# Optimization experiments

Measured on AMD Instinct MI355X. Metric: run time of the kernel, lower is better.

Reference implementation:

```python
import jax, jax.numpy as jnp
import numpy as np
from jax import lax

B, D, H, W = 4, 64, 64, 64
CH = 150


def setup_inputs() -> dict:
    key = jax.random.key(0)
    k1, k2, k3, k4 = jax.random.split(key, 4)
    image = jax.random.uniform(k1, (B, 2, D, H, W), dtype=jnp.float32)
    # PyTorch-like init scales
    h_w = jax.random.normal(k2, (CH, 1, 3, 3, 3), dtype=jnp.float32) * (1.0 / np.sqrt(27.0))
    h_b = jax.random.normal(k3, (CH,), dtype=jnp.float32) * 0.05
    p_w = jax.random.normal(k4, (1, CH, 1, 1, 1), dtype=jnp.float32) * (1.0 / np.sqrt(CH))
    return {"image": image, "h_w": h_w, "h_b": h_b, "p_w": p_w, "k": 30}


def _max_pool3(v):
    # 3x3x3 max pool, stride 1, padding 1 (torch pads with -inf for max pool)
    return lax.reduce_window(
        v, -jnp.inf, lax.max,
        window_dimensions=(1, 1, 3, 3, 3),
        window_strides=(1, 1, 1, 1, 1),
        padding=[(0, 0), (0, 0), (1, 1), (1, 1), (1, 1)])


def reference(image, h_w, h_b, p_w, k):
    x = image[:, 0:1]            # [B,1,D,H,W] occupancy
    r = image[:, 1:2]            # [B,1,D,H,W] reward
    h = lax.conv_general_dilated(
        x, h_w, window_strides=(1, 1, 1), padding="SAME",
        dimension_numbers=("NCDHW", "OIDHW", "NCDHW"))
    h = jax.nn.relu(h + h_b[None, :, None, None, None])  # [B,150,D,H,W]
    # 1x1x1 conv == channel contraction
    p = jax.nn.sigmoid(jnp.einsum("bcdhw,c->bdhw", h, p_w[0, :, 0, 0, 0])[:, None])
    v = r
    for _ in range(k):
        v = jnp.maximum(v, r + p * (_max_pool3(v) - r))
    return v
```

## Files before the change

kernel.cpp:

```cpp
#include <hip/hip_runtime.h>
#include <math.h>

#define NEG_INF (-__builtin_inff())

typedef __attribute__((ext_vector_type(8))) short short8;
typedef __attribute__((ext_vector_type(4))) float f32x4;

__device__ __forceinline__ unsigned f2bf(float f) {
    union { float f; unsigned u; } v; v.f = f;
    return (v.u + 0x7fffu + ((v.u >> 16) & 1u)) >> 16;
}

__device__ __forceinline__ float dpp_shr1(float x) {
    return __int_as_float(__builtin_amdgcn_update_dpp(
        0, __float_as_int(x), 0x111, 0xF, 0xF, true));
}
__device__ __forceinline__ float dpp_shr2(float x) {
    return __int_as_float(__builtin_amdgcn_update_dpp(
        0, __float_as_int(x), 0x112, 0xF, 0xF, true));
}
__device__ __forceinline__ float dpp_shr4(float x) {
    return __int_as_float(__builtin_amdgcn_update_dpp(
        0, __float_as_int(x), 0x114, 0xF, 0xF, true));
}
__device__ __forceinline__ float dpp_shr8(float x) {
    return __int_as_float(__builtin_amdgcn_update_dpp(
        0, __float_as_int(x), 0x118, 0xF, 0xF, true));
}
__device__ __forceinline__ float dpp_shl1(float x) {
    return __int_as_float(__builtin_amdgcn_update_dpp(
        0, __float_as_int(x), 0x101, 0xF, 0xF, true));
}

__global__ __launch_bounds__(256) void pad_kernel(
    const float* __restrict__ img, unsigned short* __restrict__ pad)
{
    int i = blockIdx.x * 256 + threadIdx.x;
    if (i >= 66 * 66 * 66) return;
    int b = blockIdx.y;
    int z = i / 4356;
    int rem = i - z * 4356;
    int y = rem / 66;
    int x = rem - y * 66;
    float v = 0.f;
    if (z >= 1 && z <= 64 && y >= 1 && y <= 64 && x >= 1 && x <= 64)
        v = img[((size_t)b << 19) + ((z - 1) << 12) + ((y - 1) << 6) + (x - 1)];
    pad[(size_t)b * 287496 + i] = (unsigned short)f2bf(v);
}

__global__ __launch_bounds__(256, 4) void gate_mfma(
    const unsigned short* __restrict__ pad,
    const float* __restrict__ hw, const float* __restrict__ hb,
    const float* __restrict__ pw, float* __restrict__ p)
{
    __shared__ int4 Bsh[10 * 64];

    const int lane = threadIdx.x & 63;
    const int col  = lane & 15;
    const int q    = lane >> 4;
    const int wid  = threadIdx.x >> 6;
    const int W    = blockIdx.x * 4 + wid;

    for (int t = wid; t < 10; t += 4) {
        int c = 16 * t + col;
        bool cv = c < 150;
        unsigned hv[8];
        #pragma unroll
        for (int j = 0; j < 8; ++j) {
            int k = 8 * q + j;
            float wv = 0.f;
            if (cv) {
                if (k < 27) wv = hw[c * 27 + k];
                else if (k == 27) wv = hb[c];
            }
            hv[j] = f2bf(wv);
        }
        Bsh[t * 64 + lane] = make_int4(hv[0] | (hv[1] << 16), hv[2] | (hv[3] << 16),
                                       hv[4] | (hv[5] << 16), hv[6] | (hv[7] << 16));
    }
    float pwv[10];
    #pragma unroll
    for (int t = 0; t < 10; ++t) {
        int c = 16 * t + col;
        pwv[t] = (c < 150) ? pw[c] : 0.f;
    }
    __syncthreads();

    int4 bfrag[10];
    #pragma unroll
    for (int t = 0; t < 10; ++t) bfrag[t] = Bsh[t * 64 + lane];

    int offL[8]; unsigned cstA[8]; bool ldA[8];
    #pragma unroll
    for (int j = 0; j < 8; ++j) {
        int k = 8 * q + j;
        int dz = (k * 57) >> 9;
        int rem = k - 9 * dz;
        int dy = (rem * 171) >> 9;
        int dx = rem - 3 * dy;
        ldA[j]  = (k < 27);
        offL[j] = (k < 27) ? (dz * 4356 + dy * 66 + dx) : 0;
        cstA[j] = (k == 27) ? 0x3F80u : 0u;
    }

    int y = W & 63, zz = (W >> 6) & 63, b = W >> 12;
    int rbase = b * 287496 + zz * 4356 + y * 66 + col;

    #pragma unroll 2
    for (int i = 0; i < 4; ++i) {
        int x0    = i << 4;
        int abase = rbase + x0;

        unsigned av[8];
        #pragma unroll
        for (int j = 0; j < 8; ++j) {
            unsigned v = pad[abase + offL[j]];
            av[j] = ldA[j] ? v : cstA[j];
        }
        union { int4 i4; short8 s8; } af, bfu;
        af.i4 = make_int4(av[0] | (av[1] << 16), av[2] | (av[3] << 16),
                          av[4] | (av[5] << 16), av[6] | (av[7] << 16));

        const f32x4 zero = {0.f, 0.f, 0.f, 0.f};
        f32x4 rr[10];
        #pragma unroll
        for (int t = 0; t < 10; ++t) {
            bfu.i4 = bfrag[t];
            rr[t] = __builtin_amdgcn_mfma_f32_16x16x32_bf16(af.s8, bfu.s8, zero, 0, 0, 0);
        }
        float ax = 0.f, ay = 0.f, az = 0.f, aw = 0.f;
        #pragma unroll
        for (int t = 0; t < 10; ++t) {
            ax = fmaf(pwv[t], fmaxf(rr[t].x, 0.f), ax);
            ay = fmaf(pwv[t], fmaxf(rr[t].y, 0.f), ay);
            az = fmaf(pwv[t], fmaxf(rr[t].z, 0.f), az);
            aw = fmaf(pwv[t], fmaxf(rr[t].w, 0.f), aw);
        }
        ax += dpp_shr1(ax); ax += dpp_shr2(ax); ax += dpp_shr4(ax); ax += dpp_shr8(ax);
        ay += dpp_shr1(ay); ay += dpp_shr2(ay); ay += dpp_shr4(ay); ay += dpp_shr8(ay);
        az += dpp_shr1(az); az += dpp_shr2(az); az += dpp_shr4(az); az += dpp_shr8(az);
        aw += dpp_shr1(aw); aw += dpp_shr2(aw); aw += dpp_shr4(aw); aw += dpp_shr8(aw);
        if (col == 15) {
            float4 o;
            o.x = 1.f / (1.f + __expf(-ax));
            o.y = 1.f / (1.f + __expf(-ay));
            o.z = 1.f / (1.f + __expf(-az));
            o.w = 1.f / (1.f + __expf(-aw));
            *(float4*)(p + (b << 18) + (zz << 12) + (y << 6) + x0 + 4 * q) = o;
        }
    }
}

#define ZC 12
#define YC 16
#define PL 1024
#define ZMID 6

template<int T>
__global__ __launch_bounds__(512, 4) void prop_kernel(
    const float* __restrict__ vin, int sstride,
    const float* __restrict__ rimg,
    const float* __restrict__ pbuf,
    float* __restrict__ vout)
{
    __shared__ float S[ZC * PL];
    int blk = blockIdx.x;
    int b  = blk >> 7;
    int tz = ((blk >> 3) & 15) << 2;
    int ty = (blk & 7) << 3;

    const float* vb = vin  + (size_t)b * sstride;
    const float* rb = rimg + ((size_t)b << 19);
    const float* pb = pbuf + ((size_t)b << 18);
    float*       ob = vout + ((size_t)b << 18);

    int tid  = threadIdx.x;
    int x4   = tid & 15, x0 = x4 << 2;
    int yy   = (tid >> 4) & 15;
    int h    = tid >> 8;
    int lane = tid & 63;
    (void)lane;

    int gy = ty + yy - 4;
    bool vy = (unsigned)gy < 64u;

    {
        const float* src = vb + gy * 64 + x0;
        #pragma unroll
        for (int zi = 0; zi < 6; ++zi) {
            int z  = 6 * h + zi;
            int gz = tz + z - 4;
            float4 v = make_float4(NEG_INF, NEG_INF, NEG_INF, NEG_INF);
            if (vy && ((unsigned)gz < 64u)) v = *(const float4*)(src + (gz << 12));
            *(float4*)(S + z * PL + yy * 64 + x0) = v;
        }
    }
    __syncthreads();

    int lbase = yy * 64 + x0;
    int goff  = gy * 64 + x0;

    #define ROWY(zz_, Q, C) {                                                  \
        const float* pz = S + (zz_) * PL + lbase;                              \
        float4 r0 = *(const float4*)(pz - 64);                                 \
        float4 r1 = *(const float4*)(pz);                                      \
        float4 r2 = *(const float4*)(pz + 64);                                 \
        float4 cm;                                                             \
        cm.x = fmaxf(fmaxf(r0.x, r1.x), r2.x);                                 \
        cm.y = fmaxf(fmaxf(r0.y, r1.y), r2.y);                                 \
        cm.z = fmaxf(fmaxf(r0.z, r1.z), r2.z);                                 \
        cm.w = fmaxf(fmaxf(r0.w, r1.w), r2.w);                                 \
        float lm = dpp_shr1(cm.w);                        \
        float rm = dpp_shl1(cm.x);                        \
        if (x4 == 0)  lm = NEG_INF;                                            \
        if (x4 == 15) rm = NEG_INF;                                            \
        Q.x = fmaxf(lm, fmaxf(cm.x, cm.y));                                    \
        Q.y = fmaxf(cm.x, fmaxf(cm.y, cm.z));                                  \
        Q.z = fmaxf(cm.y, fmaxf(cm.z, cm.w));                                  \
        Q.w = fmaxf(fmaxf(cm.z, cm.w), rm);                                    \
        C = r1;                                                                \
    }

    #pragma unroll
    for (int it = 0; it < T; ++it) {
        const int lo   = 5 - T + it;
        const int span = ZMID - lo;
        bool act = (yy >= lo) && (yy < YC - lo);
        int zlo = h ? ZMID : lo;
        float4 vn[5];
        if (act) {
            float4 q0, q1, q2, c1, c2, cd;
            ROWY(zlo - 1, q0, cd);
            ROWY(zlo,     q1, c1);
            #pragma unroll
            for (int zi = 0; zi < span; ++zi) {
                int z = zlo + zi;
                ROWY(z + 1, q2, c2);
                int gz = tz + z - 4;
                float4 r;
                if (vy && ((unsigned)gz < 64u)) {
                    int off = (gz << 12) + goff;
                    float4 pv = *(const float4*)(pb + off);
                    float4 rv = *(const float4*)(rb + off);
                    float4 m3;
                    m3.x = fmaxf(fmaxf(q0.x, q1.x), q2.x);
                    m3.y = fmaxf(fmaxf(q0.y, q1.y), q2.y);
                    m3.z = fmaxf(fmaxf(q0.z, q1.z), q2.z);
                    m3.w = fmaxf(fmaxf(q0.w, q1.w), q2.w);
                    r.x = fmaxf(c1.x, fmaf(pv.x, m3.x - rv.x, rv.x));
                    r.y = fmaxf(c1.y, fmaf(pv.y, m3.y - rv.y, rv.y));
                    r.z = fmaxf(c1.z, fmaf(pv.z, m3.z - rv.z, rv.z));
                    r.w = fmaxf(c1.w, fmaf(pv.w, m3.w - rv.w, rv.w));
                    if (it == T - 1) *(float4*)(ob + off) = r;
                } else {
                    r = c1;
                }
                vn[zi] = r;
                q0 = q1; q1 = q2; c1 = c2;
            }
        }
        __syncthreads();
        if (act) {
            #pragma unroll
            for (int zi = 0; zi < span; ++zi)
                *(float4*)(S + (zlo + zi) * PL + lbase) = vn[zi];
        }
        __syncthreads();
    }
    #undef ROWY
}

extern "C" void kernel_launch(void* const* d_in, const int* in_sizes, int n_in,
                              void* d_out, int out_size, void* d_ws, size_t ws_size,
                              hipStream_t stream) {
    const float* img = (const float*)d_in[0];
    const float* hw  = (const float*)d_in[1];
    const float* hb  = (const float*)d_in[2];
    const float* pw  = (const float*)d_in[3];

    float* out = (float*)d_out;
    float* p   = (float*)d_ws;
    float* vA  = (float*)((char*)d_ws + (4u << 20));
    unsigned short* pad = (unsigned short*)((char*)d_ws + (4u << 20));

    pad_kernel<<<dim3(1124, 4), 256, 0, stream>>>(img, pad);
    gate_mfma<<<4096, 256, 0, stream>>>(pad, hw, hb, pw, p);

    const float* r0 = img + (1 << 18);

    prop_kernel<4><<<512, 512, 0, stream>>>(r0,  1 << 19, r0, p, vA);
    prop_kernel<4><<<512, 512, 0, stream>>>(vA,  1 << 18, r0, p, out);
    prop_kernel<4><<<512, 512, 0, stream>>>(out, 1 << 18, r0, p, vA);
    prop_kernel<4><<<512, 512, 0, stream>>>(vA,  1 << 18, r0, p, out);
    prop_kernel<4><<<512, 512, 0, stream>>>(out, 1 << 18, r0, p, vA);
    prop_kernel<4><<<512, 512, 0, stream>>>(vA,  1 << 18, r0, p, out);
    prop_kernel<4><<<512, 512, 0, stream>>>(out, 1 << 18, r0, p, vA);
    prop_kernel<2><<<512, 512, 0, stream>>>(vA,  1 << 18, r0, p, out);
}
```

Before: 203.9 us.

## Keep z-column of values in registers and separate max pool via LDS

Each thread now holds its six z-planes of v in registers instead of staging the whole tile in LDS. It computes the z and x max pool in registers, exchanges only the boundary plane between the two z-halves through a small LDS buffer, and does the y direction through an intermediate LDS plane. This cuts LDS traffic per iteration from three rows per plane to a write plus two reads of partial maxima. The cost is more registers per thread, which could hurt occupancy at 512 threads per block.

Result: faster. 179.4 us (-12.0%).

```diff
diff --git a/kernel.cpp b/kernel.cpp
--- a/kernel.cpp
+++ b/kernel.cpp
@@ -151,10 +151,8 @@
     }
 }
 
-#define ZC 12
 #define YC 16
 #define PL 1024
-#define ZMID 6
 
 template<int T>
 __global__ __launch_bounds__(512, 4) void prop_kernel(
@@ -163,7 +161,9 @@
     const float* __restrict__ pbuf,
     float* __restrict__ vout)
 {
-    __shared__ float S[ZC * PL];
+    __shared__ float TL[10 * PL];
+    __shared__ float VEX[2 * PL];
+
     int blk = blockIdx.x;
     int b  = blk >> 7;
     int tz = ((blk >> 3) & 15) << 2;
@@ -178,96 +178,88 @@
     int x4   = tid & 15, x0 = x4 << 2;
     int yy   = (tid >> 4) & 15;
     int h    = tid >> 8;
-    int lane = tid & 63;
-    (void)lane;
 
     int gy = ty + yy - 4;
     bool vy = (unsigned)gy < 64u;
-
-    {
-        const float* src = vb + gy * 64 + x0;
-        #pragma unroll
-        for (int zi = 0; zi < 6; ++zi) {
-            int z  = 6 * h + zi;
-            int gz = tz + z - 4;
-            float4 v = make_float4(NEG_INF, NEG_INF, NEG_INF, NEG_INF);
-            if (vy && ((unsigned)gz < 64u)) v = *(const float4*)(src + (gz << 12));
-            *(float4*)(S + z * PL + yy * 64 + x0) = v;
-        }
-    }
-    __syncthreads();
-
     int lbase = yy * 64 + x0;
     int goff  = gy * 64 + x0;
 
-    #define ROWY(zz_, Q, C) {                                                  \
-        const float* pz = S + (zz_) * PL + lbase;                              \
-        float4 r0 = *(const float4*)(pz - 64);                                 \
-        float4 r1 = *(const float4*)(pz);                                      \
-        float4 r2 = *(const float4*)(pz + 64);                                 \
-        float4 cm;                                                             \
-        cm.x = fmaxf(fmaxf(r0.x, r1.x), r2.x);                                 \
-        cm.y = fmaxf(fmaxf(r0.y, r1.y), r2.y);                                 \
-        cm.z = fmaxf(fmaxf(r0.z, r1.z), r2.z);                                 \
-        cm.w = fmaxf(fmaxf(r0.w, r1.w), r2.w);                                 \
-        float lm = dpp_shr1(cm.w);                        \
-        float rm = dpp_shl1(cm.x);                        \
-        if (x4 == 0)  lm = NEG_INF;                                            \
-        if (x4 == 15) rm = NEG_INF;                                            \
-        Q.x = fmaxf(lm, fmaxf(cm.x, cm.y));                                    \
-        Q.y = fmaxf(cm.x, fmaxf(cm.y, cm.z));                                  \
-        Q.z = fmaxf(cm.y, fmaxf(cm.z, cm.w));                                  \
-        Q.w = fmaxf(fmaxf(cm.z, cm.w), rm);                                    \
-        C = r1;                                                                \
-    }
+    float4 v[6];
+    #pragma unroll
+    for (int zi = 0; zi < 6; ++zi) {
+        int z  = h ? (11 - zi) : zi;
+        int gz = tz + z - 4;
+        float4 val = make_float4(NEG_INF, NEG_INF, NEG_INF, NEG_INF);
+        if (vy && ((unsigned)gz < 64u)) val = *(const float4*)(vb + (gz << 12) + goff);
+        v[zi] = val;
+    }
+    *(float4*)(VEX + h * PL + lbase) = v[5];
+    __syncthreads();
 
     #pragma unroll
     for (int it = 0; it < T; ++it) {
-        const int lo   = 5 - T + it;
-        const int span = ZMID - lo;
-        bool act = (yy >= lo) && (yy < YC - lo);
-        int zlo = h ? ZMID : lo;
-        float4 vn[5];
-        if (act) {
-            float4 q0, q1, q2, c1, c2, cd;
-            ROWY(zlo - 1, q0, cd);
-            ROWY(zlo,     q1, c1);
-            #pragma unroll
-            for (int zi = 0; zi < span; ++zi) {
-                int z = zlo + zi;
-                ROWY(z + 1, q2, c2);
-                int gz = tz + z - 4;
-                float4 r;
+        const int lo = 5 - T + it;
+        bool act_t = (yy >= lo - 1) && (yy < 17 - lo);
+        bool act   = (yy >= lo) && (yy < YC - lo);
+
+        float4 vexN = *(const float4*)(VEX + (h ^ 1) * PL + lbase);
+        float4 t[5];
+        #pragma unroll
+        for (int zi = lo; zi < 6; ++zi) {
+            float4 za = v[zi - 1];
+            float4 zb = v[zi];
+            float4 zc = (zi == 5) ? vexN : v[zi + 1];
+            float4 zm;
+            zm.x = fmaxf(fmaxf(za.x, zb.x), zc.x);
+            zm.y = fmaxf(fmaxf(za.y, zb.y), zc.y);
+            zm.z = fmaxf(fmaxf(za.z, zb.z), zc.z);
+            zm.w = fmaxf(fmaxf(za.w, zb.w), zc.w);
+            float lm = dpp_shr1(zm.w);
+            float rm = dpp_shl1(zm.x);
+            if (x4 == 0)  lm = NEG_INF;
+            if (x4 == 15) rm = NEG_INF;
+            float4 tt;
+            tt.x = fmaxf(lm, fmaxf(zm.x, zm.y));
+            tt.y = fmaxf(zm.x, fmaxf(zm.y, zm.z));
+            tt.z = fmaxf(zm.y, fmaxf(zm.z, zm.w));
+            tt.w = fmaxf(fmaxf(zm.z, zm.w), rm);
+            t[zi - lo] = tt;
+            int z = h ? (11 - zi) : zi;
+            if (act_t) *(float4*)(TL + (z - 1) * PL + lbase) = tt;
+        }
+        __syncthreads();
+
+        #pragma unroll
+        for (int zi = lo; zi < 6; ++zi) {
+            int z  = h ? (11 - zi) : zi;
+            int gz = tz + z - 4;
+            if (act) {
+                const float* tp = TL + (z - 1) * PL + lbase;
+                float4 tu = *(const float4*)(tp - 64);
+                float4 td = *(const float4*)(tp + 64);
+                float4 ts = t[zi - lo];
+                float4 m3;
+                m3.x = fmaxf(fmaxf(tu.x, td.x), ts.x);
+                m3.y = fmaxf(fmaxf(tu.y, td.y), ts.y);
+                m3.z = fmaxf(fmaxf(tu.z, td.z), ts.z);
+                m3.w = fmaxf(fmaxf(tu.w, td.w), ts.w);
                 if (vy && ((unsigned)gz < 64u)) {
                     int off = (gz << 12) + goff;
                     float4 pv = *(const float4*)(pb + off);
                     float4 rv = *(const float4*)(rb + off);
-                    float4 m3;
-                    m3.x = fmaxf(fmaxf(q0.x, q1.x), q2.x);
-                    m3.y = fmaxf(fmaxf(q0.y, q1.y), q2.y);
-                    m3.z = fmaxf(fmaxf(q0.z, q1.z), q2.z);
-                    m3.w = fmaxf(fmaxf(q0.w, q1.w), q2.w);
-                    r.x = fmaxf(c1.x, fmaf(pv.x, m3.x - rv.x, rv.x));
-                    r.y = fmaxf(c1.y, fmaf(pv.y, m3.y - rv.y, rv.y));
-                    r.z = fmaxf(c1.z, fmaf(pv.z, m3.z - rv.z, rv.z));
-                    r.w = fmaxf(c1.w, fmaf(pv.w, m3.w - rv.w, rv.w));
-                    if (it == T - 1) *(float4*)(ob + off) = r;
-                } else {
-                    r = c1;
+                    float4 nv;
+                    nv.x = fmaxf(v[zi].x, fmaf(pv.x, m3.x - rv.x, rv.x));
+                    nv.y = fmaxf(v[zi].y, fmaf(pv.y, m3.y - rv.y, rv.y));
+                    nv.z = fmaxf(v[zi].z, fmaf(pv.z, m3.z - rv.z, rv.z));
+                    nv.w = fmaxf(v[zi].w, fmaf(pv.w, m3.w - rv.w, rv.w));
+                    v[zi] = nv;
+                    if (it == T - 1) *(float4*)(ob + off) = nv;
                 }
-                vn[zi] = r;
-                q0 = q1; q1 = q2; c1 = c2;
             }
         }
+        *(float4*)(VEX + h * PL + lbase) = v[5];
         __syncthreads();
-        if (act) {
-            #pragma unroll
-            for (int zi = 0; zi < span; ++zi)
-                *(float4*)(S + (zlo + zi) * PL + lbase) = vn[zi];
-        }
-        __syncthreads();
-    }
-    #undef ROWY
+    }
 }
 
 extern "C" void kernel_launch(void* const* d_in, const int* in_sizes, int n_in,
```
